# Kernel tuning notes

Measured on AMD Instinct MI355X. Metric: run time of the kernel, lower is better.

## Reference

```python
import jax, jax.numpy as jnp
import numpy as np

B, L, N, DOUT = 8, 8192, 256, 256  # batch, seq_len, state_dim, output_dim


def setup_inputs() -> dict:
    key = jax.random.key(0)
    k_u, k_h, k_w = jax.random.split(key, 3)
    u = jax.random.normal(k_u, (B, L, 1), dtype=jnp.float32)
    # impulse response buffer (stands in for A_bar^i @ B_bar rows); decay-scaled for realism
    h = jax.random.normal(k_h, (L, N), dtype=jnp.float32) * 0.02
    W = jax.random.normal(k_w, (DOUT, N), dtype=jnp.float32) * (1.0 / np.sqrt(N))
    return {"u": u, "h": h, "W": W}


def reference(u, h, W):
    L_ = h.shape[0]
    n_fft = 2 * L_
    # FFT-based long convolution: U:[B, n_fft//2+1, 1], H:[n_fft//2+1, N]
    U = jnp.fft.rfft(u, n=n_fft, axis=1)
    H = jnp.fft.rfft(h, n=n_fft, axis=0)
    M = U * H[None, :, :]                      # broadcast channel 1 -> N
    m = jnp.fft.irfft(M, n=n_fft, axis=1)[:, :L_, :]  # [B, L, N]
    return jnp.einsum('bln,on->blo', m, W)     # Linear(state_dim -> output_dim), no bias
```

## Files before the change

### kernel.cpp

```cpp
#include <hip/hip_runtime.h>
#include <hip/hip_bf16.h>
#include <stdint.h>
#include <stddef.h>

typedef __attribute__((ext_vector_type(4))) float f32x4;
typedef __attribute__((ext_vector_type(8))) short s16x8;

#define B_    8
#define L_    8192
#define N_    256
#define DOUT_ 256

__device__ __forceinline__ unsigned short f2bf(float f) {
  unsigned int x = __float_as_uint(f);
  x += 0x7fff + ((x >> 16) & 1);
  return (unsigned short)(x >> 16);
}

__global__ void k_amat(const float* __restrict__ u, unsigned short* __restrict__ Am) {
  int t = blockIdx.x * 256 + threadIdx.x;
  int i0 = (t & 15) * 8;
  int lp = (t >> 4) & 127;
  int r2 = t >> 11;
  int d  = r2 % 65;
  int b  = r2 / 65;
  s16x8 v;
#pragma unroll
  for (int j = 0; j < 8; ++j) v[j] = 0;
  if (d < 64) {
    const float* ub = u + b * L_;
    int base = 128 * d + lp - i0;
#pragma unroll
    for (int j = 0; j < 8; ++j) {
      int idx = base - j;
      float f = (idx >= 0) ? ub[idx] : 0.0f;
      v[j] = (short)f2bf(f);
    }
  }
  *(s16x8*)(Am + (size_t)t * 8) = v;
}

__global__ void k_gt(const float* __restrict__ W, const float* __restrict__ h,
                     unsigned short* __restrict__ gT) {
  int gid  = blockIdx.x * 256 + threadIdx.x;
  int lane = gid & 63;
  int wid  = gid >> 6;
  int o_t  = wid >> 7;
  int i_t  = wid & 127;
  int o0 = o_t * 16, i0 = i_t * 64;
  int ln = lane & 15, hi = lane >> 4;
  f32x4 acc[4] = {};
#pragma unroll
  for (int k0 = 0; k0 < N_; k0 += 32) {
    const float* wp = W + (o0 + ln) * N_ + k0 + 8 * hi;
    float4 w0 = *(const float4*)wp;
    float4 w1 = *(const float4*)(wp + 4);
    s16x8 a;
    a[0] = (short)f2bf(w0.x); a[1] = (short)f2bf(w0.y);
    a[2] = (short)f2bf(w0.z); a[3] = (short)f2bf(w0.w);
    a[4] = (short)f2bf(w1.x); a[5] = (short)f2bf(w1.y);
    a[6] = (short)f2bf(w1.z); a[7] = (short)f2bf(w1.w);
#pragma unroll
    for (int ns = 0; ns < 4; ++ns) {
      const float* hp = h + (size_t)(i0 + 16 * ns + ln) * N_ + k0 + 8 * hi;
      float4 h0 = *(const float4*)hp;
      float4 h1 = *(const float4*)(hp + 4);
      s16x8 bb;
      bb[0] = (short)f2bf(h0.x); bb[1] = (short)f2bf(h0.y);
      bb[2] = (short)f2bf(h0.z); bb[3] = (short)f2bf(h0.w);
      bb[4] = (short)f2bf(h1.x); bb[5] = (short)f2bf(h1.y);
      bb[6] = (short)f2bf(h1.z); bb[7] = (short)f2bf(h1.w);
      acc[ns] = __builtin_amdgcn_mfma_f32_16x16x32_bf16(a, bb, acc[ns], 0, 0, 0);
    }
  }
#pragma unroll
  for (int ns = 0; ns < 4; ++ns)
#pragma unroll
    for (int q = 0; q < 4; ++q)
      gT[(size_t)(o0 + 4 * hi + q) * L_ + i0 + 16 * ns + ln] = f2bf(acc[ns][q]);
}

__global__ __launch_bounds__(512, 2) void k_main(const unsigned short* __restrict__ Am,
                                                 const unsigned short* __restrict__ gT,
                                                 float* __restrict__ out) {
  __shared__ short As[3][16384];
  __shared__ short Bs[3][8192];
  const int c = blockIdx.x;
  const int b = blockIdx.y;
  const int z = blockIdx.z;
  const int tid = threadIdx.x;
  const int lane = tid & 63;
  const int w = tid >> 6;
  const int wr = w >> 1, wc = w & 1;
  const int ln = lane & 15, hi = lane >> 4;
  const int ob = c * 128;

  const int t3 = tid >> 3;
  const int sA = ((tid & 7) ^ (t3 & 7)) << 3;
  const unsigned short* AmB = Am + (size_t)(b * 65) * 16384;
  const unsigned short* Bb0 = gT + (size_t)(ob + t3) * L_ + sA;
  const unsigned short* Bb1 = gT + (size_t)(ob + t3 + 64) * L_ + sA;
  const int rl0 = t3;
  const int rl1 = 64 + t3;

  const int offA = (wr * 64 + ln) * 64;
  const int offB = (wc * 64 + ln) * 64;
  const int sw = ln & 7;
  const int off_k0 = (hi ^ sw) * 8;
  const int off_k1 = ((hi + 4) ^ sw) * 8;

  float* outb = out + (size_t)b * L_ * DOUT_;

#define ISSUE_A(Rv, ktv, dst) do { \
    const int kthalf_ = (ktv) >> 1; const int kodd_ = ((ktv) & 1) << 6; \
    _Pragma("unroll") \
    for (int q = 0; q < 4; ++q) { \
      int dd = 2 * (Rv) + (q >> 1) - kthalf_; \
      int sd = dd < 0 ? 64 : dd; \
      const unsigned short* src = AmB + ((size_t)sd << 14) + ((q & 1 ? rl1 : rl0) << 7) + kodd_ + sA; \
      __builtin_amdgcn_global_load_lds((const __attribute__((address_space(1))) void*)src, \
          (__attribute__((address_space(3))) void*)((dst) + (tid + 512 * q) * 8), 16, 0, 0); \
    } \
  } while (0)

#define ISSUE_B(ktv, dst) do { \
    const int kb_ = (ktv) * 64; \
    __builtin_amdgcn_global_load_lds((const __attribute__((address_space(1))) void*)(Bb0 + kb_), \
        (__attribute__((address_space(3))) void*)((dst) + tid * 8), 16, 0, 0); \
    __builtin_amdgcn_global_load_lds((const __attribute__((address_space(1))) void*)(Bb1 + kb_), \
        (__attribute__((address_space(3))) void*)((dst) + (tid + 512) * 8), 16, 0, 0); \
  } while (0)

  auto run_section = [&](const int R) {
    short *ar = &As[0][0], *an = &As[1][0], *aw = &As[2][0];
    short *br = &Bs[0][0], *bn = &Bs[1][0], *bw = &Bs[2][0];
    f32x4 acc[4][4] = {};
    const int nkt = 4 * (R + 1);

    ISSUE_A(R, 0, ar); ISSUE_B(0, br);
    ISSUE_A(R, 1, an); ISSUE_B(1, bn);

    for (int kt = 0; kt < nkt; ++kt) {
      asm volatile("s_waitcnt vmcnt(6)" ::: "memory");
      __builtin_amdgcn_sched_barrier(0);
      __builtin_amdgcn_s_barrier();
      __builtin_amdgcn_sched_barrier(0);

      const int kt2 = (kt + 2 < nkt) ? kt + 2 : nkt - 1;

      s16x8 af[4][2], bf[2][2];
#pragma unroll
      for (int m = 0; m < 4; ++m) {
        af[m][0] = *(const s16x8*)(ar + offA + m * 1024 + off_k0);
        af[m][1] = *(const s16x8*)(ar + offA + m * 1024 + off_k1);
      }
#pragma unroll
      for (int n = 0; n < 2; ++n) {
        bf[n][0] = *(const s16x8*)(br + offB + n * 1024 + off_k0);
        bf[n][1] = *(const s16x8*)(br + offB + n * 1024 + off_k1);
      }
      ISSUE_A(R, kt2, aw);
      __builtin_amdgcn_s_setprio(1);
#pragma unroll
      for (int kk = 0; kk < 2; ++kk)
#pragma unroll
        for (int m = 0; m < 4; ++m)
#pragma unroll
          for (int n = 0; n < 2; ++n)
            acc[m][n] = __builtin_amdgcn_mfma_f32_16x16x32_bf16(af[m][kk], bf[n][kk], acc[m][n], 0, 0, 0);
      __builtin_amdgcn_s_setprio(0);

      s16x8 bg[2][2];
#pragma unroll
      for (int n = 0; n < 2; ++n) {
        bg[n][0] = *(const s16x8*)(br + offB + (n + 2) * 1024 + off_k0);
        bg[n][1] = *(const s16x8*)(br + offB + (n + 2) * 1024 + off_k1);
      }
      ISSUE_B(kt2, bw);
      __builtin_amdgcn_s_setprio(1);
#pragma unroll
      for (int kk = 0; kk < 2; ++kk)
#pragma unroll
        for (int m = 0; m < 4; ++m)
#pragma unroll
          for (int n = 0; n < 2; ++n)
            acc[m][n + 2] = __builtin_amdgcn_mfma_f32_16x16x32_bf16(af[m][kk], bg[n][kk], acc[m][n + 2], 0, 0, 0);
      __builtin_amdgcn_s_setprio(0);

      short* t;
      t = ar; ar = an; an = aw; aw = t;
      t = br; br = bn; bn = bw; bw = t;
    }

    __builtin_amdgcn_s_barrier();
    asm volatile("s_waitcnt vmcnt(0)" ::: "memory");

    const int l0 = R * 256 + wr * 64 + 4 * hi;
    const int o0 = ob + wc * 64 + ln;
#pragma unroll
    for (int m = 0; m < 4; ++m)
#pragma unroll
      for (int q = 0; q < 4; ++q) {
        float* rowp = outb + (size_t)(l0 + m * 16 + q) * DOUT_ + o0;
#pragma unroll
        for (int n = 0; n < 4; ++n)
          rowp[n * 16] = acc[m][n][q];
      }
  };

  run_section(31 - z);
  run_section(z);

#undef ISSUE_A
#undef ISSUE_B
}

extern "C" void kernel_launch(void* const* d_in, const int* in_sizes, int n_in,
                              void* d_out, int out_size, void* d_ws, size_t ws_size,
                              hipStream_t stream) {
  const float* u = (const float*)d_in[0];
  const float* h = (const float*)d_in[1];
  const float* W = (const float*)d_in[2];
  float* out = (float*)d_out;

  char* ws = (char*)d_ws;
  const size_t AM_BYTES = (size_t)8 * 65 * 16384 * 2;
  unsigned short* Am = (unsigned short*)ws;
  unsigned short* gT = (unsigned short*)(ws + AM_BYTES);

  k_amat<<<4160, 256, 0, stream>>>(u, Am);
  k_gt<<<512, 256, 0, stream>>>(W, h, gT);
  k_main<<<dim3(2, 8, 16), 512, 0, stream>>>(Am, gT, out);
}
```

Before: 176.7 us.

## Split paired causal sections across two blocks with full-width tiles and atomic merge

The main GEMM now gives each block all 256 output columns (256x256 tile, 8 waves as 2x4) and splits the combined work of the paired sections (31-z and z, 132 k-steps in total) evenly between two blocks. The block that straddles the boundary flushes partial results with atomicAdd into the upper half of the output, which a new kernel zeroes first. A new pre-pass also reverses and converts u to bf16 once, so k_amat only gathers shorts. This balances the per-block work and halves the A-tile reloads, but it adds atomics, an extra zeroing pass over half the output, a double buffer in place of the triple buffer, and a full vmcnt(0) wait on every step.

```diff
diff --git a/kernel.cpp b/kernel.cpp
--- a/kernel.cpp
+++ b/kernel.cpp
@@ -17,7 +17,24 @@
   return (unsigned short)(x >> 16);
 }
 
-__global__ void k_amat(const float* __restrict__ u, unsigned short* __restrict__ Am) {
+__global__ void k_zero(float* __restrict__ out) {
+  int t = blockIdx.x * 256 + threadIdx.x;
+  int b = t >> 18;
+  int r = t & 262143;
+  f32x4 z = {0.f, 0.f, 0.f, 0.f};
+  *(f32x4*)(out + (size_t)b * 2097152 + 1048576 + (size_t)r * 4) = z;
+}
+
+__global__ void k_urev(const float* __restrict__ u, unsigned short* __restrict__ urev) {
+  int t = blockIdx.x * 256 + threadIdx.x;
+  int b = t >> 14;
+  int j = t & 16383;
+  unsigned short v = 0;
+  if (j <= 8191) v = f2bf(u[b * L_ + 8191 - j]);
+  urev[t] = v;
+}
+
+__global__ void k_amat(const unsigned short* __restrict__ urev, unsigned short* __restrict__ Am) {
   int t = blockIdx.x * 256 + threadIdx.x;
   int i0 = (t & 15) * 8;
   int lp = (t >> 4) & 127;
@@ -28,14 +45,10 @@
 #pragma unroll
   for (int j = 0; j < 8; ++j) v[j] = 0;
   if (d < 64) {
-    const float* ub = u + b * L_;
-    int base = 128 * d + lp - i0;
-#pragma unroll
-    for (int j = 0; j < 8; ++j) {
-      int idx = base - j;
-      float f = (idx >= 0) ? ub[idx] : 0.0f;
-      v[j] = (short)f2bf(f);
-    }
+    const unsigned short* ur = urev + b * 16384;
+    int jbase = 8191 - 128 * d - lp + i0;
+#pragma unroll
+    for (int j = 0; j < 8; ++j) v[j] = (short)ur[jbase + j];
   }
   *(s16x8*)(Am + (size_t)t * 8) = v;
 }
@@ -83,133 +96,152 @@
 __global__ __launch_bounds__(512, 2) void k_main(const unsigned short* __restrict__ Am,
                                                  const unsigned short* __restrict__ gT,
                                                  float* __restrict__ out) {
-  __shared__ short As[3][16384];
-  __shared__ short Bs[3][8192];
-  const int c = blockIdx.x;
-  const int b = blockIdx.y;
-  const int z = blockIdx.z;
+  __shared__ short As[2][16384];
+  __shared__ short Bs[2][16384];
+  const int half = blockIdx.x;
+  const int b    = blockIdx.y;
+  const int zp   = blockIdx.z;
+  const int Rb = 31 - zp, Rs = zp;
+  const int nktb = 4 * (Rb + 1);
+  const int s_lo = half ? 66 : 0;
+  const int s_hi = half ? 132 : 66;
   const int tid = threadIdx.x;
   const int lane = tid & 63;
   const int w = tid >> 6;
-  const int wr = w >> 1, wc = w & 1;
+  const int wr = w >> 2, wc = w & 3;
   const int ln = lane & 15, hi = lane >> 4;
-  const int ob = c * 128;
 
   const int t3 = tid >> 3;
   const int sA = ((tid & 7) ^ (t3 & 7)) << 3;
   const unsigned short* AmB = Am + (size_t)(b * 65) * 16384;
-  const unsigned short* Bb0 = gT + (size_t)(ob + t3) * L_ + sA;
-  const unsigned short* Bb1 = gT + (size_t)(ob + t3 + 64) * L_ + sA;
-  const int rl0 = t3;
-  const int rl1 = 64 + t3;
-
-  const int offA = (wr * 64 + ln) * 64;
+  const unsigned short* Bq[4] = {
+    gT + (size_t)(t3)       * L_ + sA,
+    gT + (size_t)(t3 + 64)  * L_ + sA,
+    gT + (size_t)(t3 + 128) * L_ + sA,
+    gT + (size_t)(t3 + 192) * L_ + sA };
+  const int rl0 = t3, rl1 = 64 + t3;
+
+  const int offA = (wr * 128 + ln) * 64;
   const int offB = (wc * 64 + ln) * 64;
   const int sw = ln & 7;
-  const int off_k0 = (hi ^ sw) * 8;
-  const int off_k1 = ((hi + 4) ^ sw) * 8;
-
-  float* outb = out + (size_t)b * L_ * DOUT_;
-
-#define ISSUE_A(Rv, ktv, dst) do { \
-    const int kthalf_ = (ktv) >> 1; const int kodd_ = ((ktv) & 1) << 6; \
-    _Pragma("unroll") \
-    for (int q = 0; q < 4; ++q) { \
-      int dd = 2 * (Rv) + (q >> 1) - kthalf_; \
-      int sd = dd < 0 ? 64 : dd; \
-      const unsigned short* src = AmB + ((size_t)sd << 14) + ((q & 1 ? rl1 : rl0) << 7) + kodd_ + sA; \
-      __builtin_amdgcn_global_load_lds((const __attribute__((address_space(1))) void*)src, \
-          (__attribute__((address_space(3))) void*)((dst) + (tid + 512 * q) * 8), 16, 0, 0); \
-    } \
+  const int k0o = (hi ^ sw) * 8;
+  const int k1o = ((hi + 4) ^ sw) * 8;
+
+  float* outb = out + (size_t)b * (L_ * DOUT_);
+  f32x4 acc[8][4] = {};
+
+#define ISSUE_A(Rv, ktv, dst, q) do { \
+    int dd = 2 * (Rv) + ((q) >> 1) - ((ktv) >> 1); \
+    int sd = dd < 0 ? 64 : dd; \
+    const unsigned short* src = AmB + ((size_t)sd << 14) + (((q) & 1 ? rl1 : rl0) << 7) + (((ktv) & 1) << 6) + sA; \
+    __builtin_amdgcn_global_load_lds((const __attribute__((address_space(1))) void*)src, \
+        (__attribute__((address_space(3))) void*)((dst) + (tid + 512 * (q)) * 8), 16, 0, 0); \
   } while (0)
 
-#define ISSUE_B(ktv, dst) do { \
-    const int kb_ = (ktv) * 64; \
-    __builtin_amdgcn_global_load_lds((const __attribute__((address_space(1))) void*)(Bb0 + kb_), \
-        (__attribute__((address_space(3))) void*)((dst) + tid * 8), 16, 0, 0); \
-    __builtin_amdgcn_global_load_lds((const __attribute__((address_space(1))) void*)(Bb1 + kb_), \
-        (__attribute__((address_space(3))) void*)((dst) + (tid + 512) * 8), 16, 0, 0); \
+#define ISSUE_B(ktv, dst, q) do { \
+    const unsigned short* src = Bq[q] + (ktv) * 64; \
+    __builtin_amdgcn_global_load_lds((const __attribute__((address_space(1))) void*)src, \
+        (__attribute__((address_space(3))) void*)((dst) + (tid + 512 * (q)) * 8), 16, 0, 0); \
   } while (0)
 
-  auto run_section = [&](const int R) {
-    short *ar = &As[0][0], *an = &As[1][0], *aw = &As[2][0];
-    short *br = &Bs[0][0], *bn = &Bs[1][0], *bw = &Bs[2][0];
-    f32x4 acc[4][4] = {};
-    const int nkt = 4 * (R + 1);
-
-    ISSUE_A(R, 0, ar); ISSUE_B(0, br);
-    ISSUE_A(R, 1, an); ISSUE_B(1, bn);
-
-    for (int kt = 0; kt < nkt; ++kt) {
-      asm volatile("s_waitcnt vmcnt(6)" ::: "memory");
-      __builtin_amdgcn_sched_barrier(0);
-      __builtin_amdgcn_s_barrier();
-      __builtin_amdgcn_sched_barrier(0);
-
-      const int kt2 = (kt + 2 < nkt) ? kt + 2 : nkt - 1;
-
-      s16x8 af[4][2], bf[2][2];
-#pragma unroll
-      for (int m = 0; m < 4; ++m) {
-        af[m][0] = *(const s16x8*)(ar + offA + m * 1024 + off_k0);
-        af[m][1] = *(const s16x8*)(ar + offA + m * 1024 + off_k1);
-      }
-#pragma unroll
-      for (int n = 0; n < 2; ++n) {
-        bf[n][0] = *(const s16x8*)(br + offB + n * 1024 + off_k0);
-        bf[n][1] = *(const s16x8*)(br + offB + n * 1024 + off_k1);
-      }
-      ISSUE_A(R, kt2, aw);
-      __builtin_amdgcn_s_setprio(1);
-#pragma unroll
-      for (int kk = 0; kk < 2; ++kk)
-#pragma unroll
-        for (int m = 0; m < 4; ++m)
-#pragma unroll
-          for (int n = 0; n < 2; ++n)
-            acc[m][n] = __builtin_amdgcn_mfma_f32_16x16x32_bf16(af[m][kk], bf[n][kk], acc[m][n], 0, 0, 0);
-      __builtin_amdgcn_s_setprio(0);
-
-      s16x8 bg[2][2];
-#pragma unroll
-      for (int n = 0; n < 2; ++n) {
-        bg[n][0] = *(const s16x8*)(br + offB + (n + 2) * 1024 + off_k0);
-        bg[n][1] = *(const s16x8*)(br + offB + (n + 2) * 1024 + off_k1);
-      }
-      ISSUE_B(kt2, bw);
-      __builtin_amdgcn_s_setprio(1);
-#pragma unroll
-      for (int kk = 0; kk < 2; ++kk)
-#pragma unroll
-        for (int m = 0; m < 4; ++m)
-#pragma unroll
-          for (int n = 0; n < 2; ++n)
-            acc[m][n + 2] = __builtin_amdgcn_mfma_f32_16x16x32_bf16(af[m][kk], bg[n][kk], acc[m][n + 2], 0, 0, 0);
-      __builtin_amdgcn_s_setprio(0);
-
-      short* t;
-      t = ar; ar = an; an = aw; aw = t;
-      t = br; br = bn; bn = bw; bw = t;
-    }
-
-    __builtin_amdgcn_s_barrier();
-    asm volatile("s_waitcnt vmcnt(0)" ::: "memory");
-
-    const int l0 = R * 256 + wr * 64 + 4 * hi;
-    const int o0 = ob + wc * 64 + ln;
-#pragma unroll
-    for (int m = 0; m < 4; ++m)
+  auto flush = [&](int R, bool atomic) {
+    const int l0 = R * 256 + wr * 128 + 4 * hi;
+    const int o0 = wc * 64 + ln;
+#pragma unroll
+    for (int m = 0; m < 8; ++m)
 #pragma unroll
       for (int q = 0; q < 4; ++q) {
         float* rowp = outb + (size_t)(l0 + m * 16 + q) * DOUT_ + o0;
 #pragma unroll
-        for (int n = 0; n < 4; ++n)
-          rowp[n * 16] = acc[m][n][q];
+        for (int n = 0; n < 4; ++n) {
+          if (atomic) atomicAdd(rowp + n * 16, acc[m][n][q]);
+          else        rowp[n * 16] = acc[m][n][q];
+        }
       }
+#pragma unroll
+    for (int m = 0; m < 8; ++m)
+#pragma unroll
+      for (int n = 0; n < 4; ++n)
+        acc[m][n] = (f32x4){0.f, 0.f, 0.f, 0.f};
   };
 
-  run_section(31 - z);
-  run_section(z);
+  {
+    short* Aw = &As[s_lo & 1][0];
+    short* Bw = &Bs[s_lo & 1][0];
+    const int kt0 = s_lo;
+    ISSUE_A(Rb, kt0, Aw, 0); ISSUE_A(Rb, kt0, Aw, 1);
+    ISSUE_A(Rb, kt0, Aw, 2); ISSUE_A(Rb, kt0, Aw, 3);
+    ISSUE_B(kt0, Bw, 0); ISSUE_B(kt0, Bw, 1);
+    ISSUE_B(kt0, Bw, 2); ISSUE_B(kt0, Bw, 3);
+  }
+
+  for (int s = s_lo; s < s_hi; ++s) {
+    asm volatile("s_waitcnt vmcnt(0)" ::: "memory");
+    __builtin_amdgcn_sched_barrier(0);
+    __builtin_amdgcn_s_barrier();
+    __builtin_amdgcn_sched_barrier(0);
+
+    if (half && s == nktb) flush(Rb, true);
+
+    const short* Ac = &As[s & 1][0];
+    const short* Bc = &Bs[s & 1][0];
+    short* Aw = &As[(s + 1) & 1][0];
+    short* Bw = &Bs[(s + 1) & 1][0];
+    const int s1  = (s + 1 < s_hi) ? s + 1 : s;
+    const int R1  = (s1 < nktb) ? Rb : Rs;
+    const int kt1 = (s1 < nktb) ? s1 : s1 - nktb;
+
+    s16x8 bf[4], af[4];
+#pragma unroll
+    for (int n = 0; n < 4; ++n) bf[n] = *(const s16x8*)(Bc + offB + n * 1024 + k0o);
+    ISSUE_A(R1, kt1, Aw, 0); ISSUE_A(R1, kt1, Aw, 1);
+#pragma unroll
+    for (int m = 0; m < 4; ++m) af[m] = *(const s16x8*)(Ac + offA + m * 1024 + k0o);
+    __builtin_amdgcn_s_setprio(1);
+#pragma unroll
+    for (int m = 0; m < 4; ++m)
+#pragma unroll
+      for (int n = 0; n < 4; ++n)
+        acc[m][n] = __builtin_amdgcn_mfma_f32_16x16x32_bf16(af[m], bf[n], acc[m][n], 0, 0, 0);
+    __builtin_amdgcn_s_setprio(0);
+    ISSUE_A(R1, kt1, Aw, 2); ISSUE_A(R1, kt1, Aw, 3);
+#pragma unroll
+    for (int m = 0; m < 4; ++m) af[m] = *(const s16x8*)(Ac + offA + 4096 + m * 1024 + k0o);
+    __builtin_amdgcn_s_setprio(1);
+#pragma unroll
+    for (int m = 0; m < 4; ++m)
+#pragma unroll
+      for (int n = 0; n < 4; ++n)
+        acc[4 + m][n] = __builtin_amdgcn_mfma_f32_16x16x32_bf16(af[m], bf[n], acc[4 + m][n], 0, 0, 0);
+    __builtin_amdgcn_s_setprio(0);
+#pragma unroll
+    for (int n = 0; n < 4; ++n) bf[n] = *(const s16x8*)(Bc + offB + n * 1024 + k1o);
+    ISSUE_B(kt1, Bw, 0); ISSUE_B(kt1, Bw, 1);
+#pragma unroll
+    for (int m = 0; m < 4; ++m) af[m] = *(const s16x8*)(Ac + offA + m * 1024 + k1o);
+    __builtin_amdgcn_s_setprio(1);
+#pragma unroll
+    for (int m = 0; m < 4; ++m)
+#pragma unroll
+      for (int n = 0; n < 4; ++n)
+        acc[m][n] = __builtin_amdgcn_mfma_f32_16x16x32_bf16(af[m], bf[n], acc[m][n], 0, 0, 0);
+    __builtin_amdgcn_s_setprio(0);
+    ISSUE_B(kt1, Bw, 2); ISSUE_B(kt1, Bw, 3);
+#pragma unroll
+    for (int m = 0; m < 4; ++m) af[m] = *(const s16x8*)(Ac + offA + 4096 + m * 1024 + k1o);
+    __builtin_amdgcn_s_setprio(1);
+#pragma unroll
+    for (int m = 0; m < 4; ++m)
+#pragma unroll
+      for (int n = 0; n < 4; ++n)
+        acc[4 + m][n] = __builtin_amdgcn_mfma_f32_16x16x32_bf16(af[m], bf[n], acc[4 + m][n], 0, 0, 0);
+    __builtin_amdgcn_s_setprio(0);
+  }
+
+  asm volatile("s_waitcnt vmcnt(0)" ::: "memory");
+
+  if (half) flush(Rs, false);
+  else      flush(Rb, true);
 
 #undef ISSUE_A
 #undef ISSUE_B
@@ -225,10 +257,13 @@
 
   char* ws = (char*)d_ws;
   const size_t AM_BYTES = (size_t)8 * 65 * 16384 * 2;
-  unsigned short* Am = (unsigned short*)ws;
-  unsigned short* gT = (unsigned short*)(ws + AM_BYTES);
-
-  k_amat<<<4160, 256, 0, stream>>>(u, Am);
+  unsigned short* Am   = (unsigned short*)ws;
+  unsigned short* gT   = (unsigned short*)(ws + AM_BYTES);
+  unsigned short* urev = (unsigned short*)(ws + AM_BYTES + (size_t)4 * 1024 * 1024);
+
+  k_zero<<<8192, 256, 0, stream>>>(out);
+  k_urev<<<512, 256, 0, stream>>>(u, urev);
+  k_amat<<<4160, 256, 0, stream>>>(urev, Am);
   k_gt<<<512, 256, 0, stream>>>(W, h, gT);
   k_main<<<dim3(2, 8, 16), 512, 0, stream>>>(Am, gT, out);
 }
```

New measurement: 188.2 us. 6.5% more time.
